# Optimization experiments

Measured on AMD Instinct MI355X. Metric: run time of the kernel, lower is better.

Reference implementation:

```python
import jax, jax.numpy as jnp
import numpy as np

ALPHA = 0.3
B, T = 512, 65536


def setup_inputs() -> dict:
    key = jax.random.key(0)
    # F0 values roughly in a vocal pitch range; uniform fill per spec
    f0_frames = jax.random.uniform(key, (B, T), dtype=jnp.float32)
    return {"f0_frames": f0_frames}


def reference(f0_frames):
    # EMA: y[t] = alpha*x[t] + (1-alpha)*y[t-1], with y_prev initialized to x[:,0]
    # (so y[0] == x[0], matching the torch loop).
    alpha = jnp.float32(ALPHA)
    one_m_alpha = jnp.float32(1.0 - ALPHA)
    x_t = jnp.swapaxes(f0_frames, 0, 1)  # (T, B) for scan over time

    def step(carry, x):
        y = alpha * x + one_m_alpha * carry
        return y, y

    _, ys = jax.lax.scan(step, x_t[0], x_t)  # ys: (T, B)
    return jnp.swapaxes(ys, 0, 1)  # (B, T)
```

## Files before the change

### kernel.cpp

```cpp
#include <hip/hip_runtime.h>


#define EMA_ALPHA 0.3f
#define EMA_BETA  0.7f
#define BLOCK 256
#define R     32
#define TILE  (BLOCK * R)
#define K     64

__device__ __forceinline__ int skew(int i) { return i + (i >> 5); }

__global__ __launch_bounds__(BLOCK) void ema_kernel(
    const float* __restrict__ x, float* __restrict__ y,
    int T, int tilesPerRow) {
  __shared__ float lds[TILE + K + ((TILE + K) >> 5) + 1];

  const int tid      = threadIdx.x;
  const int row      = blockIdx.x / tilesPerRow;
  const int tile     = blockIdx.x % tilesPerRow;
  const int tile_t0  = tile * TILE;
  const float* xrow  = x + (size_t)row * (size_t)T;
  float*       yrow  = y + (size_t)row * (size_t)T;

  const int NV = (TILE + K) / 4;
  for (int p4 = tid; p4 < NV; p4 += BLOCK) {
    const int p = p4 * 4;
    const int t = tile_t0 - K + p;
    if (t >= 0) {
      const float4 v = *reinterpret_cast<const float4*>(xrow + t);
      lds[skew(p    )] = v.x;
      lds[skew(p + 1)] = v.y;
      lds[skew(p + 2)] = v.z;
      lds[skew(p + 3)] = v.w;
    }
  }
  __syncthreads();

  const int t0 = tile_t0 + tid * R;
  const int s  = (t0 - K > 0) ? (t0 - K) : 0;
  int ps = s - tile_t0 + K;
  float carry = lds[skew(ps)];
  const int nwu = t0 - 1 - s;
  for (int it = 0; it < nwu; ++it) {
    ++ps;
    carry = fmaf(EMA_ALPHA, lds[skew(ps)], EMA_BETA * carry);
  }
  __syncthreads();

  const int p0 = K + tid * R;
#pragma unroll
  for (int j = 0; j < R; ++j) {
    const float v = lds[skew(p0 + j)];
    carry = fmaf(EMA_ALPHA, v, EMA_BETA * carry);
    lds[skew(p0 + j)] = carry;
  }
  __syncthreads();

  for (int p4 = tid; p4 < TILE / 4; p4 += BLOCK) {
    const int p = p4 * 4;
    float4 v;
    v.x = lds[skew(K + p    )];
    v.y = lds[skew(K + p + 1)];
    v.z = lds[skew(K + p + 2)];
    v.w = lds[skew(K + p + 3)];
    *reinterpret_cast<float4*>(yrow + tile_t0 + p) = v;
  }
}

extern "C" void kernel_launch(void* const* d_in, const int* in_sizes, int n_in,
                              void* d_out, int out_size, void* d_ws, size_t ws_size,
                              hipStream_t stream) {
  const float* x = (const float*)d_in[0];
  float* y = (float*)d_out;

  const int T = 65536;
  const int B = in_sizes[0] / T;
  const int tilesPerRow = T / TILE;
  const int grid = B * tilesPerRow;

  ema_kernel<<<grid, BLOCK, 0, stream>>>(x, y, T, tilesPerRow);
}
```

Before: 53.18 us.

## Store EMA results from registers with nontemporal stores, halve tile and warm-up

Each thread now keeps its scanned outputs in registers and writes them straight to global memory with nontemporal vector stores. This removes the write-back into shared memory, the separate coalesced store pass and two block barriers. Per-thread run length and warm-up window are both halved, and the warm-up loop is fully unrolled in the common case. In exchange, the stores are strided across lanes rather than contiguous, and the shorter warm-up truncates the recurrence earlier, which slightly increases numerical error.

```diff
diff --git a/kernel.cpp b/kernel.cpp
--- a/kernel.cpp
+++ b/kernel.cpp
@@ -4,9 +4,11 @@
 #define EMA_ALPHA 0.3f
 #define EMA_BETA  0.7f
 #define BLOCK 256
-#define R     32
+#define R     16
 #define TILE  (BLOCK * R)
-#define K     64
+#define K     32
+
+typedef float floatx4 __attribute__((ext_vector_type(4)));
 
 __device__ __forceinline__ int skew(int i) { return i + (i >> 5); }
 
@@ -37,33 +39,39 @@
   __syncthreads();
 
   const int t0 = tile_t0 + tid * R;
-  const int s  = (t0 - K > 0) ? (t0 - K) : 0;
-  int ps = s - tile_t0 + K;
-  float carry = lds[skew(ps)];
-  const int nwu = t0 - 1 - s;
-  for (int it = 0; it < nwu; ++it) {
-    ++ps;
-    carry = fmaf(EMA_ALPHA, lds[skew(ps)], EMA_BETA * carry);
+  float c;
+  if (t0 - K > 0) {
+    const int ps = tid * R;
+    c = lds[skew(ps)];
+#pragma unroll
+    for (int it = 1; it < K; ++it) {
+      c = fmaf(EMA_ALPHA, lds[skew(ps + it)], EMA_BETA * c);
+    }
+  } else {
+    const int s  = 0;
+    int ps = s - tile_t0 + K;
+    ps = K + s - tile_t0 - K + 0;
+    ps = s + K - tile_t0;
+    ps = K;
+    c = lds[skew(ps)];
+    const int nwu = t0 - 1;
+    for (int it = 0; it < nwu; ++it) {
+      ++ps;
+      c = fmaf(EMA_ALPHA, lds[skew(ps)], EMA_BETA * c);
+    }
   }
-  __syncthreads();
 
   const int p0 = K + tid * R;
+  floatx4 o[R / 4];
 #pragma unroll
   for (int j = 0; j < R; ++j) {
-    const float v = lds[skew(p0 + j)];
-    carry = fmaf(EMA_ALPHA, v, EMA_BETA * carry);
-    lds[skew(p0 + j)] = carry;
+    c = fmaf(EMA_ALPHA, lds[skew(p0 + j)], EMA_BETA * c);
+    reinterpret_cast<float*>(o)[j] = c;
   }
-  __syncthreads();
-
-  for (int p4 = tid; p4 < TILE / 4; p4 += BLOCK) {
-    const int p = p4 * 4;
-    float4 v;
-    v.x = lds[skew(K + p    )];
-    v.y = lds[skew(K + p + 1)];
-    v.z = lds[skew(K + p + 2)];
-    v.w = lds[skew(K + p + 3)];
-    *reinterpret_cast<float4*>(yrow + tile_t0 + p) = v;
+#pragma unroll
+  for (int q = 0; q < R / 4; ++q) {
+    __builtin_nontemporal_store(o[q],
+        reinterpret_cast<floatx4*>(yrow + t0 + q * 4));
   }
 }
 
```

New measurement: 107.5 us. 2.02x slower.

## Replace LDS tiled EMA with register chunks and shuffle-based carry combine

Applied to the files above, without the earlier changes.

Each thread now loads 16 contiguous elements straight into registers and runs a local EMA from zero. It then builds its incoming carry from the three preceding lanes' chunk-end values, read with warp shuffles and weighted by precomputed powers of 0.7; lanes 0-2 fall back to a short 32-element recompute from global memory. The carry is folded back in with fmas against a power table, and results go out with nontemporal stores. This drops the LDS staging, the barriers and the long 64-step warmup, at the cost of truncating the carry contribution to a finite window, which relies on 0.7^48 being negligible.

```diff
diff --git a/kernel.cpp b/kernel.cpp
--- a/kernel.cpp
+++ b/kernel.cpp
@@ -1,70 +1,80 @@
 #include <hip/hip_runtime.h>
 
 
-#define EMA_ALPHA 0.3f
-#define EMA_BETA  0.7f
+#define AL 0.3f
+#define BE 0.7f
 #define BLOCK 256
-#define R     32
-#define TILE  (BLOCK * R)
-#define K     64
+#define RPT 16
+#define F16 0.0033232930569601f
+#define F32 1.10450644586e-05f
 
-__device__ __forceinline__ int skew(int i) { return i + (i >> 5); }
+typedef float floatx4 __attribute__((ext_vector_type(4)));
 
 __global__ __launch_bounds__(BLOCK) void ema_kernel(
     const float* __restrict__ x, float* __restrict__ y,
     int T, int tilesPerRow) {
-  __shared__ float lds[TILE + K + ((TILE + K) >> 5) + 1];
+  const int tid     = threadIdx.x;
+  const int lane    = tid & 63;
+  const int tile_t0 = (blockIdx.x % tilesPerRow) * (BLOCK * RPT);
+  const int t0      = tile_t0 + (tid >> 6) * (64 * RPT) + lane * RPT;
+  const size_t rowoff = (size_t)(blockIdx.x / tilesPerRow) * (size_t)T;
+  const float* xrow = x + rowoff;
+  float*       yrow = y + rowoff;
 
-  const int tid      = threadIdx.x;
-  const int row      = blockIdx.x / tilesPerRow;
-  const int tile     = blockIdx.x % tilesPerRow;
-  const int tile_t0  = tile * TILE;
-  const float* xrow  = x + (size_t)row * (size_t)T;
-  float*       yrow  = y + (size_t)row * (size_t)T;
+  const float* px = xrow + t0;
+  floatx4 a0 = *(const floatx4*)(px);
+  floatx4 a1 = *(const floatx4*)(px + 4);
+  floatx4 a2 = *(const floatx4*)(px + 8);
+  floatx4 a3 = *(const floatx4*)(px + 12);
+  const float x0 = a0[0];
 
-  const int NV = (TILE + K) / 4;
-  for (int p4 = tid; p4 < NV; p4 += BLOCK) {
-    const int p = p4 * 4;
-    const int t = tile_t0 - K + p;
-    if (t >= 0) {
-      const float4 v = *reinterpret_cast<const float4*>(xrow + t);
-      lds[skew(p    )] = v.x;
-      lds[skew(p + 1)] = v.y;
-      lds[skew(p + 2)] = v.z;
-      lds[skew(p + 3)] = v.w;
-    }
+  float c = 0.f;
+#define STEP(v, i) c = fmaf(AL, (v)[i], BE * c); (v)[i] = c;
+  STEP(a0,0) STEP(a0,1) STEP(a0,2) STEP(a0,3)
+  STEP(a1,0) STEP(a1,1) STEP(a1,2) STEP(a1,3)
+  STEP(a2,0) STEP(a2,1) STEP(a2,2) STEP(a2,3)
+  STEP(a3,0) STEP(a3,1) STEP(a3,2) STEP(a3,3)
+#undef STEP
+  const float lend = c;
+
+  const float s1 = __shfl_up(lend, 1, 64);
+  const float s2 = __shfl_up(lend, 2, 64);
+  const float s3 = __shfl_up(lend, 3, 64);
+
+  float cin;
+  if (lane >= 3) {
+    cin = fmaf(F16, s2, fmaf(F32, s3, s1));
+  } else if (t0 == 0) {
+    cin = x0;
+  } else if (t0 >= 32) {
+    const float* ph = xrow + t0 - 32;
+    float cc = 0.f;
+#pragma unroll 8
+    for (int k = 0; k < 32; ++k) cc = fmaf(AL, ph[k], BE * cc);
+    cin = cc;
+  } else {
+    float cc = xrow[0];
+    for (int t = 1; t < t0; ++t) cc = fmaf(AL, xrow[t], BE * cc);
+    cin = cc;
   }
-  __syncthreads();
 
-  const int t0 = tile_t0 + tid * R;
-  const int s  = (t0 - K > 0) ? (t0 - K) : 0;
-  int ps = s - tile_t0 + K;
-  float carry = lds[skew(ps)];
-  const int nwu = t0 - 1 - s;
-  for (int it = 0; it < nwu; ++it) {
-    ++ps;
-    carry = fmaf(EMA_ALPHA, lds[skew(ps)], EMA_BETA * carry);
-  }
-  __syncthreads();
+  const float P[16] = {
+    0.7f, 0.49f, 0.343f, 0.2401f,
+    0.16807f, 0.117649f, 0.0823543f, 0.05764801f,
+    0.040353607f, 0.0282475249f, 0.019773267f, 0.013841287f,
+    0.009688901f, 0.0067822307f, 0.0047475615f, 0.0033232931f };
+#define CMB(v, i, j) (v)[i] = fmaf(cin, P[j], (v)[i]);
+  CMB(a0,0,0)  CMB(a0,1,1)  CMB(a0,2,2)  CMB(a0,3,3)
+  CMB(a1,0,4)  CMB(a1,1,5)  CMB(a1,2,6)  CMB(a1,3,7)
+  CMB(a2,0,8)  CMB(a2,1,9)  CMB(a2,2,10) CMB(a2,3,11)
+  CMB(a3,0,12) CMB(a3,1,13) CMB(a3,2,14) CMB(a3,3,15)
+#undef CMB
 
-  const int p0 = K + tid * R;
-#pragma unroll
-  for (int j = 0; j < R; ++j) {
-    const float v = lds[skew(p0 + j)];
-    carry = fmaf(EMA_ALPHA, v, EMA_BETA * carry);
-    lds[skew(p0 + j)] = carry;
-  }
-  __syncthreads();
-
-  for (int p4 = tid; p4 < TILE / 4; p4 += BLOCK) {
-    const int p = p4 * 4;
-    float4 v;
-    v.x = lds[skew(K + p    )];
-    v.y = lds[skew(K + p + 1)];
-    v.z = lds[skew(K + p + 2)];
-    v.w = lds[skew(K + p + 3)];
-    *reinterpret_cast<float4*>(yrow + tile_t0 + p) = v;
-  }
+  float* py = yrow + t0;
+  __builtin_nontemporal_store(a0, (floatx4*)(py));
+  __builtin_nontemporal_store(a1, (floatx4*)(py + 4));
+  __builtin_nontemporal_store(a2, (floatx4*)(py + 8));
+  __builtin_nontemporal_store(a3, (floatx4*)(py + 12));
 }
 
 extern "C" void kernel_launch(void* const* d_in, const int* in_sizes, int n_in,
@@ -75,7 +85,7 @@
 
   const int T = 65536;
   const int B = in_sizes[0] / T;
-  const int tilesPerRow = T / TILE;
+  const int tilesPerRow = T / (BLOCK * RPT);
   const int grid = B * tilesPerRow;
 
   ema_kernel<<<grid, BLOCK, 0, stream>>>(x, y, T, tilesPerRow);
```

Result: slower. 98.56 us (+85.3%).
